# Kernel tuning notes

Hardware: AMD Instinct MI355X
Metric: run time of the kernel (lower is better)

Reference implementation:

```python
import jax, jax.numpy as jnp
import numpy as np

K = 3        # patch size (size=(3,3))
DIL = 1      # dilation
EPS = 1e-8


def _unfold(x, k=K, d=DIL):
    """im2col identical to torch.nn.Unfold(kernel_size=k, dilation=d).
    x: [N, C, H, W] -> [N, C*k*k, L], channel-major then (kh, kw) ordering."""
    N, C, H, W = x.shape
    Ho = H - d * (k - 1)
    Wo = W - d * (k - 1)
    rows = []
    for i in range(k):
        cols = [x[:, :, i * d:i * d + Ho, j * d:j * d + Wo] for j in range(k)]
        rows.append(jnp.stack(cols, axis=2))  # [N, C, k, Ho, Wo]
    patches = jnp.stack(rows, axis=2)         # [N, C, k, k, Ho, Wo]
    return patches.reshape(N, C * k * k, Ho * Wo)


def setup_inputs() -> dict:
    key = jax.random.key(0)
    k1, k2 = jax.random.split(key)
    x = jax.random.normal(k1, (1, 256, 96, 96), dtype=jnp.float32)
    style = jax.random.normal(k2, (1, 256, 96, 96), dtype=jnp.float32)
    return {"x": x, "style": style}


def reference(x, style):
    # Patches of input and style feature maps: [B, D, L] with D = C*3*3.
    ip = _unfold(x)       # [B, D, Li]
    sp = _unfold(style)   # [B, D, Ls]  (precomputed in __init__ in the torch module)

    # Normalized cross-correlation between every input patch and every style patch.
    ipn = ip / (jnp.linalg.norm(ip, axis=1, keepdims=True) + EPS)
    spn = sp / (jnp.linalg.norm(sp, axis=1, keepdims=True) + EPS)
    sim = jnp.einsum('bdi,bdj->bij', ipn, spn)  # [B, Li, Ls]

    # Nearest style patch for each input patch (Champandard patch matching).
    idx = jnp.argmax(sim, axis=2)                                  # [B, Li]
    matched = jnp.take_along_axis(sp, idx[:, None, :], axis=2)     # [B, D, Li]

    # MSE between input patches and their best-matching style patches.
    return jnp.mean((ip - matched) ** 2)
```

## Files before the change

### kernel.cpp

```cpp
#include <hip/hip_runtime.h>

#define CCH   256
#define HH    96
#define WW    96
#define HO    94
#define LL    8836
#define DD    2304
#define LPAD  8960

#define BM2   256
#define NT2   35
#define NPH   36
#define ASLB  16384
#define BBASEB 65536

typedef unsigned char u8;
typedef unsigned long long u64;

using i32x4 = __attribute__((ext_vector_type(4))) int;

#define OFF_BQ    20643840ull
#define OFF_RNB   41287680ull
#define OFF_N2B   41323520ull
#define OFF_W2X   41359360ull
#define OFF_QSA   41395200ull
#define OFF_QSB   41431040ull
#define OFF_COLS  41466880ull
#define OFF_SAF   41502720ull
#define OFF_P2    41538560ull
#define OFF_PM    41612288ull
#define OFF_BEST  41686016ull

__device__ __forceinline__ void gload16(const void* g, void* l) {
    __builtin_amdgcn_global_load_lds(
        (const __attribute__((address_space(1))) unsigned int*)g,
        (__attribute__((address_space(3))) unsigned int*)l,
        16, 0, 0);
}

__global__ __launch_bounds__(256) void k_chan_stats(const float* __restrict__ st,
                                                    const float* __restrict__ x,
                                                    float* __restrict__ P2,
                                                    float* __restrict__ PM) {
    int p = blockIdx.x * 256 + threadIdx.x;
    if (p >= 2 * HH * WW) return;
    const float* img = (p < HH * WW) ? st : x;
    int pp = (p < HH * WW) ? p : p - HH * WW;
    float s = 0.f, m = 0.f;
#pragma unroll 4
    for (int c = 0; c < CCH; ++c) {
        float v = img[c * (HH * WW) + pp];
        s += v * v;
        m = fmaxf(m, fabsf(v));
    }
    P2[p] = s;
    PM[p] = m;
}

__global__ __launch_bounds__(256) void k_win(const float* __restrict__ P2,
                                             const float* __restrict__ PM,
                                             float* __restrict__ rnB,
                                             float* __restrict__ n2B,
                                             float* __restrict__ win2x,
                                             float* __restrict__ qsA,
                                             float* __restrict__ qsB,
                                             float* __restrict__ colS,
                                             float* __restrict__ sAf) {
    int i = blockIdx.x * 256 + threadIdx.x;
    if (i >= LL) return;
    int y = i / HO, xc = i % HO;
    float ss = 0.f, sx = 0.f, ms = 0.f, mx = 0.f;
#pragma unroll
    for (int kh = 0; kh < 3; ++kh)
#pragma unroll
        for (int kw = 0; kw < 3; ++kw) {
            int off = (y + kh) * WW + xc + kw;
            ss += P2[off];
            sx += P2[HH * WW + off];
            ms = fmaxf(ms, PM[off]);
            mx = fmaxf(mx, PM[HH * WW + off]);
        }
    float rn = 1.f / (sqrtf(ss) + 1e-8f);
    float msc = fmaxf(ms, 1e-30f), mxc = fmaxf(mx, 1e-30f);
    rnB[i] = rn;
    n2B[i] = ss;
    win2x[i] = sx;
    qsA[i] = 127.f / mxc;
    qsB[i] = 127.f / msc;
    colS[i] = rn * msc * (1.f / 127.f);
    sAf[i] = mxc * (1.f / 127.f);
}

__global__ __launch_bounds__(512) void k_pack(const float* __restrict__ x,
                                              const float* __restrict__ st,
                                              const float* __restrict__ qsA,
                                              const float* __restrict__ qsB,
                                              u8* __restrict__ Aq,
                                              u8* __restrict__ Bq) {
    extern __shared__ u8 plds[];

    const int b = blockIdx.x;
    const int side = b & 1;
    const int half = (b >> 1) & 1;
    const int y = b >> 2;
    const int xc0 = half * 47;

    const float* src = side ? st : x;
    const float* qs  = side ? qsB : qsA;
    u8* dst = (side ? Bq : Aq) + (size_t)(y * HO + xc0) * DD;

    const int t = threadIdx.x;
    if (t < 47 * 9) {
        const int il = t / 9, k = t - il * 9;
        const int kh = k / 3, kw = k - kh * 3;
        const int i = y * HO + xc0 + il;
        const float scale = qs[i];
        const float* sp = src + (y + kh) * WW + (xc0 + il + kw);
        u8* lp = plds + il * DD + k;
#pragma unroll 8
        for (int c = 0; c < CCH; ++c) {
            int qv = (int)rintf(sp[c * (HH * WW)] * scale);
            lp[c * 9] = (u8)qv;
        }
    }
    __syncthreads();
    for (int idx = t; idx < 6768; idx += 512) {
        *(i32x4*)(dst + idx * 16) = *(const i32x4*)(plds + idx * 16);
    }
}

__global__ __launch_bounds__(512, 2) void k_gemm2(const u8* __restrict__ A,
                                                  const u8* __restrict__ Bm,
                                                  const float* __restrict__ colS,
                                                  u64* __restrict__ best) {
    extern __shared__ __align__(16) u8 lds[];

    const int t = threadIdx.x;
    const int wid = t >> 6, lane = t & 63;
    const int wr = wid >> 2, wc = wid & 3;
    const int l15 = lane & 15, l4 = lane >> 4;

    const int nwg = NT2 * NT2;
    const int q = nwg >> 3, r = nwg & 7;
    const int bid = blockIdx.x;
    const int xcd = bid & 7, loc = bid >> 3;
    const int swz = ((xcd < r) ? xcd * (q + 1) : r * (q + 1) + (xcd - r) * q) + loc;
    const int it = swz / NT2, jt = swz % NT2;

    const int gsrc = (t & 3) ^ ((t >> 3) & 3);
    const u8* pA0 = A  + (size_t)(it * BM2 + (t >> 2)) * DD + gsrc * 16;
    const u8* pB0 = Bm + (size_t)(jt * BM2 + (t >> 2)) * DD + gsrc * 16;

    const int sp16 = (l4 ^ ((l15 >> 1) & 3)) * 16;
    int aoff[8], boff[4];
#pragma unroll
    for (int mi = 0; mi < 8; ++mi)
        aoff[mi] = (wr * 128 + mi * 16 + l15) * 64 + sp16;
#pragma unroll
    for (int ni = 0; ni < 4; ++ni)
        boff[ni] = BBASEB + (wc * 64 + ni * 16 + l15) * 64 + sp16;

    i32x4 acc[8][4];
#pragma unroll
    for (int mi = 0; mi < 8; ++mi)
#pragma unroll
        for (int ni = 0; ni < 4; ++ni)
            acc[mi][ni] = (i32x4){0, 0, 0, 0};

#define PSTAGE(S)                                                            \
    do {                                                                     \
        const u8* sa = pA0 + (size_t)(S) * 64;                               \
        const u8* sb = pB0 + (size_t)(S) * 64;                               \
        gload16(sa,          lds + (S) * ASLB + t * 16);                     \
        gload16(sa + 294912, lds + (S) * ASLB + 8192 + t * 16);              \
        gload16(sb,          lds + BBASEB + (S) * ASLB + t * 16);            \
        gload16(sb + 294912, lds + BBASEB + (S) * ASLB + 8192 + t * 16);     \
    } while (0)
    PSTAGE(0); PSTAGE(1); PSTAGE(2);
#undef PSTAGE
    asm volatile("s_waitcnt vmcnt(8)" ::: "memory");
    __builtin_amdgcn_sched_barrier(0);
    __builtin_amdgcn_s_barrier();

    i32x4 af03[4], af47[4], bfr[4];

#define SUBA(U)                                                              \
    {                                                                        \
        _Pragma("unroll")                                                    \
        for (int ni = 0; ni < 4; ++ni)                                       \
            bfr[ni] = *(const i32x4*)(lds + (U) * ASLB + boff[ni]);          \
        _Pragma("unroll")                                                    \
        for (int mi = 0; mi < 4; ++mi)                                       \
            af03[mi] = *(const i32x4*)(lds + (U) * ASLB + aoff[mi]);         \
        {                                                                    \
            const int ss = (kb + (U) + 3 > NPH - 1) ? (NPH - 1) : (kb + (U) + 3); \
            const u8* sa = pA0 + (size_t)ss * 64;                            \
            u8* da = lds + (((U) + 3) & 3) * ASLB + t * 16;                  \
            gload16(sa,          da);                                        \
            gload16(sa + 294912, da + 8192);                                 \
        }                                                                    \
        __builtin_amdgcn_s_barrier();                                        \
        asm volatile("s_waitcnt lgkmcnt(0)" ::: "memory");                   \
        __builtin_amdgcn_sched_barrier(0);                                   \
        __builtin_amdgcn_s_setprio(1);                                       \
        _Pragma("unroll")                                                    \
        for (int mi = 0; mi < 4; ++mi)                                       \
            _Pragma("unroll")                                                \
            for (int ni = 0; ni < 4; ++ni)                                   \
                acc[mi][ni] = __builtin_amdgcn_mfma_i32_16x16x64_i8(         \
                    af03[mi], bfr[ni], acc[mi][ni], 0, 0, 0);                \
        __builtin_amdgcn_s_setprio(0);                                       \
        __builtin_amdgcn_s_barrier();                                        \
    }

#define SUBB(U)                                                              \
    {                                                                        \
        _Pragma("unroll")                                                    \
        for (int mi = 0; mi < 4; ++mi)                                       \
            af47[mi] = *(const i32x4*)(lds + (U) * ASLB + aoff[4 + mi]);     \
        {                                                                    \
            const int ss = (kb + (U) + 3 > NPH - 1) ? (NPH - 1) : (kb + (U) + 3); \
            const u8* sb = pB0 + (size_t)ss * 64;                            \
            u8* db = lds + BBASEB + (((U) + 3) & 3) * ASLB + t * 16;         \
            gload16(sb,          db);                                       \
            gload16(sb + 294912, db + 8192);                                 \
        }                                                                    \
        asm volatile("s_waitcnt vmcnt(8)" ::: "memory");                     \
        __builtin_amdgcn_sched_barrier(0);                                   \
        __builtin_amdgcn_s_barrier();                                        \
        asm volatile("s_waitcnt lgkmcnt(0)" ::: "memory");                   \
        __builtin_amdgcn_sched_barrier(0);                                   \
        __builtin_amdgcn_s_setprio(1);                                       \
        _Pragma("unroll")                                                    \
        for (int mi = 0; mi < 4; ++mi)                                       \
            _Pragma("unroll")                                                \
            for (int ni = 0; ni < 4; ++ni)                                   \
                acc[4 + mi][ni] = __builtin_amdgcn_mfma_i32_16x16x64_i8(     \
                    af47[mi], bfr[ni], acc[4 + mi][ni], 0, 0, 0);            \
        __builtin_amdgcn_s_setprio(0);                                       \
        __builtin_amdgcn_s_barrier();                                        \
    }

    for (int kt = 0; kt < NPH / 4; ++kt) {
        const int kb = kt * 4;
        SUBA(0) SUBB(0)
        SUBA(1) SUBB(1)
        SUBA(2) SUBB(2)
        SUBA(3) SUBB(3)
    }
#undef SUBA
#undef SUBB

    const int jbase = jt * BM2 + wc * 64 + l15;
    float cs[4];
#pragma unroll
    for (int ni = 0; ni < 4; ++ni) {
        int j = jbase + ni * 16;
        cs[ni] = colS[j < LL ? j : 0];
    }
#pragma unroll
    for (int mi = 0; mi < 8; ++mi) {
#pragma unroll
        for (int rr = 0; rr < 4; ++rr) {
            float bv = -3.4e38f;
            int bj = 0x7FFFFFFF;
#pragma unroll
            for (int ni = 0; ni < 4; ++ni) {
                int j = jbase + ni * 16;
                float v = (float)acc[mi][ni][rr] * cs[ni];
                if (j < LL && (v > bv || (v == bv && j < bj))) { bv = v; bj = j; }
            }
#pragma unroll
            for (int m = 1; m < 16; m <<= 1) {
                float ov = __shfl_xor(bv, m, 64);
                int oj = __shfl_xor(bj, m, 64);
                if (ov > bv || (ov == bv && oj < bj)) { bv = ov; bj = oj; }
            }
            if (l15 == 0) {
                int i = it * BM2 + wr * 128 + mi * 16 + l4 * 4 + rr;
                if (i < LL) {
                    unsigned u = __float_as_uint(bv);
                    unsigned s = (bv < 0.f) ? ~u : (u | 0x80000000u);
                    u64 packed = ((u64)s << 32) | (unsigned)(~(unsigned)bj);
                    atomicMax(&best[i], packed);
                }
            }
        }
    }
}

__global__ __launch_bounds__(256) void k_final(const u64* __restrict__ best,
                                               const float* __restrict__ rnB,
                                               const float* __restrict__ n2B,
                                               const float* __restrict__ win2x,
                                               const float* __restrict__ sAf,
                                               float* __restrict__ out) {
    int i = blockIdx.x * 256 + threadIdx.x;
    float contrib = 0.f;
    if (i < LL) {
        u64 p = best[i];
        unsigned s = (unsigned)(p >> 32);
        unsigned ub = (s & 0x80000000u) ? (s & 0x7FFFFFFFu) : ~s;
        float bv = __uint_as_float(ub);
        int j = (int)(~(unsigned)(p & 0xFFFFFFFFull));
        float dot = (bv * sAf[i]) / rnB[j];
        contrib = win2x[i] + n2B[j] - 2.f * dot;
    }
    float sred = contrib;
#pragma unroll
    for (int o = 32; o > 0; o >>= 1) sred += __shfl_down(sred, o, 64);
    __shared__ float red[4];
    if ((threadIdx.x & 63) == 0) red[threadIdx.x >> 6] = sred;
    __syncthreads();
    if (threadIdx.x == 0) {
        float tot = red[0] + red[1] + red[2] + red[3];
        atomicAdd(out, tot * (1.0f / ((float)DD * (float)LL)));
    }
}

extern "C" void kernel_launch(void* const* d_in, const int* in_sizes, int n_in,
                              void* d_out, int out_size, void* d_ws, size_t ws_size,
                              hipStream_t stream) {
    const float* x  = (const float*)d_in[0];
    const float* st = (const float*)d_in[1];
    char* ws = (char*)d_ws;

    u8* Aq       = (u8*)ws;
    u8* Bq       = (u8*)(ws + OFF_BQ);
    float* rnB   = (float*)(ws + OFF_RNB);
    float* n2B   = (float*)(ws + OFF_N2B);
    float* win2x = (float*)(ws + OFF_W2X);
    float* qsA   = (float*)(ws + OFF_QSA);
    float* qsB   = (float*)(ws + OFF_QSB);
    float* colS  = (float*)(ws + OFF_COLS);
    float* sAf   = (float*)(ws + OFF_SAF);
    float* P2    = (float*)(ws + OFF_P2);
    float* PM    = (float*)(ws + OFF_PM);
    u64* best    = (u64*)(ws + OFF_BEST);
    float* out   = (float*)d_out;

    hipFuncSetAttribute((const void*)k_gemm2,
                        hipFuncAttributeMaxDynamicSharedMemorySize, 131072);
    hipFuncSetAttribute((const void*)k_pack,
                        hipFuncAttributeMaxDynamicSharedMemorySize, 110592);

    hipMemsetAsync(best, 0, (size_t)LL * 8, stream);
    hipMemsetAsync(out, 0, sizeof(float), stream);
    hipMemsetAsync(Aq + (size_t)LL * DD, 0, (size_t)(LPAD - LL) * DD, stream);
    hipMemsetAsync(Bq + (size_t)LL * DD, 0, (size_t)(LPAD - LL) * DD, stream);

    k_chan_stats<<<dim3(72), dim3(256), 0, stream>>>(st, x, P2, PM);
    k_win<<<dim3(35), dim3(256), 0, stream>>>(P2, PM, rnB, n2B, win2x, qsA, qsB, colS, sAf);
    k_pack<<<dim3(HO * 4), dim3(512), 108288, stream>>>(x, st, qsA, qsB, Aq, Bq);
    k_gemm2<<<dim3(NT2 * NT2), dim3(512), 131072, stream>>>(Aq, Bq, colS, best);
    k_final<<<dim3(35), dim3(256), 0, stream>>>(best, rnB, n2B, win2x, sAf, out);
}
```

Baseline: 400.0 us.

## Halve GEMM M-tile, use 3-stage LDS pipeline, fold memsets into k_win

The int8 MFMA similarity GEMM moves from 256x256 tiles with a 4-stage split A/B prefetch to 128x256 tiles with a simpler 3-stage ring buffer. This cuts LDS to 72KB and accumulators to 16 per lane, so more blocks can be resident and latency is hidden better. The cost is less data reuse per tile and more global traffic for B. The best-index and output memsets are now done inside k_win, and the zeroing of the padded rows is dropped, which saves several async launches. Padded rows are safe only because their results are masked by the i<LL and j<LL checks.

```diff
diff --git a/kernel.cpp b/kernel.cpp
--- a/kernel.cpp
+++ b/kernel.cpp
@@ -8,11 +8,10 @@
 #define DD    2304
 #define LPAD  8960
 
-#define BM2   256
-#define NT2   35
+#define NTI   70
+#define NTJ   35
 #define NPH   36
-#define ASLB  16384
-#define BBASEB 65536
+#define SLTB  24576
 
 typedef unsigned char u8;
 typedef unsigned long long u64;
@@ -65,9 +64,13 @@
                                              float* __restrict__ qsA,
                                              float* __restrict__ qsB,
                                              float* __restrict__ colS,
-                                             float* __restrict__ sAf) {
+                                             float* __restrict__ sAf,
+                                             u64* __restrict__ best,
+                                             float* __restrict__ out) {
     int i = blockIdx.x * 256 + threadIdx.x;
     if (i >= LL) return;
+    if (i == 0) *out = 0.f;
+    best[i] = 0;
     int y = i / HO, xc = i % HO;
     float ss = 0.f, sx = 0.f, ms = 0.f, mx = 0.f;
 #pragma unroll
@@ -129,7 +132,7 @@
     }
 }
 
-__global__ __launch_bounds__(512, 2) void k_gemm2(const u8* __restrict__ A,
+__global__ __launch_bounds__(512, 4) void k_gemm2(const u8* __restrict__ A,
                                                   const u8* __restrict__ Bm,
                                                   const float* __restrict__ colS,
                                                   u64* __restrict__ best) {
@@ -140,65 +143,63 @@
     const int wr = wid >> 2, wc = wid & 3;
     const int l15 = lane & 15, l4 = lane >> 4;
 
-    const int nwg = NT2 * NT2;
+    const int nwg = NTI * NTJ;
     const int q = nwg >> 3, r = nwg & 7;
     const int bid = blockIdx.x;
     const int xcd = bid & 7, loc = bid >> 3;
     const int swz = ((xcd < r) ? xcd * (q + 1) : r * (q + 1) + (xcd - r) * q) + loc;
-    const int it = swz / NT2, jt = swz % NT2;
+    const int it = swz / NTJ, jt = swz % NTJ;
 
     const int gsrc = (t & 3) ^ ((t >> 3) & 3);
-    const u8* pA0 = A  + (size_t)(it * BM2 + (t >> 2)) * DD + gsrc * 16;
-    const u8* pB0 = Bm + (size_t)(jt * BM2 + (t >> 2)) * DD + gsrc * 16;
+    const u8* srcA = A  + (size_t)(it * 128 + (t >> 2)) * DD + gsrc * 16;
+    const u8* srcB = Bm + (size_t)(jt * 256 + (t >> 2)) * DD + gsrc * 16;
 
     const int sp16 = (l4 ^ ((l15 >> 1) & 3)) * 16;
-    int aoff[8], boff[4];
-#pragma unroll
-    for (int mi = 0; mi < 8; ++mi)
-        aoff[mi] = (wr * 128 + mi * 16 + l15) * 64 + sp16;
+    int aoff[4], boff[4];
+#pragma unroll
+    for (int mi = 0; mi < 4; ++mi)
+        aoff[mi] = (wr * 64 + mi * 16 + l15) * 64 + sp16;
 #pragma unroll
     for (int ni = 0; ni < 4; ++ni)
-        boff[ni] = BBASEB + (wc * 64 + ni * 16 + l15) * 64 + sp16;
-
-    i32x4 acc[8][4];
-#pragma unroll
-    for (int mi = 0; mi < 8; ++mi)
+        boff[ni] = 8192 + (wc * 64 + ni * 16 + l15) * 64 + sp16;
+
+    i32x4 acc[4][4];
+#pragma unroll
+    for (int mi = 0; mi < 4; ++mi)
 #pragma unroll
         for (int ni = 0; ni < 4; ++ni)
             acc[mi][ni] = (i32x4){0, 0, 0, 0};
 
-#define PSTAGE(S)                                                            \
+    i32x4 af[4], bf[4];
+
+#define STAGE(SS, SP)                                                        \
     do {                                                                     \
-        const u8* sa = pA0 + (size_t)(S) * 64;                               \
-        const u8* sb = pB0 + (size_t)(S) * 64;                               \
-        gload16(sa,          lds + (S) * ASLB + t * 16);                     \
-        gload16(sa + 294912, lds + (S) * ASLB + 8192 + t * 16);              \
-        gload16(sb,          lds + BBASEB + (S) * ASLB + t * 16);            \
-        gload16(sb + 294912, lds + BBASEB + (S) * ASLB + 8192 + t * 16);     \
+        const int sc_ = ((SS) > NPH - 1) ? (NPH - 1) : (SS);                 \
+        const u8* sa = srcA + (size_t)sc_ * 64;                              \
+        const u8* sb = srcB + (size_t)sc_ * 64;                              \
+        u8* d = lds + (SP) * SLTB + t * 16;                                  \
+        gload16(sa, d);                                                      \
+        gload16(sb, d + 8192);                                               \
+        gload16(sb + 128 * DD, d + 16384);                                   \
     } while (0)
-    PSTAGE(0); PSTAGE(1); PSTAGE(2);
-#undef PSTAGE
-    asm volatile("s_waitcnt vmcnt(8)" ::: "memory");
+
+    STAGE(0, 0);
+    STAGE(1, 1);
+    asm volatile("s_waitcnt vmcnt(3)" ::: "memory");
     __builtin_amdgcn_sched_barrier(0);
     __builtin_amdgcn_s_barrier();
 
-    i32x4 af03[4], af47[4], bfr[4];
-
-#define SUBA(U)                                                              \
+#define BODY(S, SC, SP)                                                      \
     {                                                                        \
         _Pragma("unroll")                                                    \
         for (int ni = 0; ni < 4; ++ni)                                       \
-            bfr[ni] = *(const i32x4*)(lds + (U) * ASLB + boff[ni]);          \
+            bf[ni] = *(const i32x4*)(lds + (SC) * SLTB + boff[ni]);          \
         _Pragma("unroll")                                                    \
         for (int mi = 0; mi < 4; ++mi)                                       \
-            af03[mi] = *(const i32x4*)(lds + (U) * ASLB + aoff[mi]);         \
-        {                                                                    \
-            const int ss = (kb + (U) + 3 > NPH - 1) ? (NPH - 1) : (kb + (U) + 3); \
-            const u8* sa = pA0 + (size_t)ss * 64;                            \
-            u8* da = lds + (((U) + 3) & 3) * ASLB + t * 16;                  \
-            gload16(sa,          da);                                        \
-            gload16(sa + 294912, da + 8192);                                 \
-        }                                                                    \
+            af[mi] = *(const i32x4*)(lds + (SC) * SLTB + aoff[mi]);          \
+        STAGE((S) + 2, SP);                                                  \
+        asm volatile("s_waitcnt vmcnt(3)" ::: "memory");                     \
+        __builtin_amdgcn_sched_barrier(0);                                   \
         __builtin_amdgcn_s_barrier();                                        \
         asm volatile("s_waitcnt lgkmcnt(0)" ::: "memory");                   \
         __builtin_amdgcn_sched_barrier(0);                                   \
@@ -208,50 +209,20 @@
             _Pragma("unroll")                                                \
             for (int ni = 0; ni < 4; ++ni)                                   \
                 acc[mi][ni] = __builtin_amdgcn_mfma_i32_16x16x64_i8(         \
-                    af03[mi], bfr[ni], acc[mi][ni], 0, 0, 0);                \
+                    af[mi], bf[ni], acc[mi][ni], 0, 0, 0);                   \
         __builtin_amdgcn_s_setprio(0);                                       \
         __builtin_amdgcn_s_barrier();                                        \
     }
 
-#define SUBB(U)                                                              \
-    {                                                                        \
-        _Pragma("unroll")                                                    \
-        for (int mi = 0; mi < 4; ++mi)                                       \
-            af47[mi] = *(const i32x4*)(lds + (U) * ASLB + aoff[4 + mi]);     \
-        {                                                                    \
-            const int ss = (kb + (U) + 3 > NPH - 1) ? (NPH - 1) : (kb + (U) + 3); \
-            const u8* sb = pB0 + (size_t)ss * 64;                            \
-            u8* db = lds + BBASEB + (((U) + 3) & 3) * ASLB + t * 16;         \
-            gload16(sb,          db);                                       \
-            gload16(sb + 294912, db + 8192);                                 \
-        }                                                                    \
-        asm volatile("s_waitcnt vmcnt(8)" ::: "memory");                     \
-        __builtin_amdgcn_sched_barrier(0);                                   \
-        __builtin_amdgcn_s_barrier();                                        \
-        asm volatile("s_waitcnt lgkmcnt(0)" ::: "memory");                   \
-        __builtin_amdgcn_sched_barrier(0);                                   \
-        __builtin_amdgcn_s_setprio(1);                                       \
-        _Pragma("unroll")                                                    \
-        for (int mi = 0; mi < 4; ++mi)                                       \
-            _Pragma("unroll")                                                \
-            for (int ni = 0; ni < 4; ++ni)                                   \
-                acc[4 + mi][ni] = __builtin_amdgcn_mfma_i32_16x16x64_i8(     \
-                    af47[mi], bfr[ni], acc[4 + mi][ni], 0, 0, 0);            \
-        __builtin_amdgcn_s_setprio(0);                                       \
-        __builtin_amdgcn_s_barrier();                                        \
-    }
-
-    for (int kt = 0; kt < NPH / 4; ++kt) {
-        const int kb = kt * 4;
-        SUBA(0) SUBB(0)
-        SUBA(1) SUBB(1)
-        SUBA(2) SUBB(2)
-        SUBA(3) SUBB(3)
-    }
-#undef SUBA
-#undef SUBB
-
-    const int jbase = jt * BM2 + wc * 64 + l15;
+    for (int s3 = 0; s3 < NPH; s3 += 3) {
+        BODY(s3,     0, 2)
+        BODY(s3 + 1, 1, 0)
+        BODY(s3 + 2, 2, 1)
+    }
+#undef BODY
+#undef STAGE
+
+    const int jbase = jt * 256 + wc * 64 + l15;
     float cs[4];
 #pragma unroll
     for (int ni = 0; ni < 4; ++ni) {
@@ -259,7 +230,7 @@
         cs[ni] = colS[j < LL ? j : 0];
     }
 #pragma unroll
-    for (int mi = 0; mi < 8; ++mi) {
+    for (int mi = 0; mi < 4; ++mi) {
 #pragma unroll
         for (int rr = 0; rr < 4; ++rr) {
             float bv = -3.4e38f;
@@ -277,7 +248,7 @@
                 if (ov > bv || (ov == bv && oj < bj)) { bv = ov; bj = oj; }
             }
             if (l15 == 0) {
-                int i = it * BM2 + wr * 128 + mi * 16 + l4 * 4 + rr;
+                int i = it * 128 + wr * 64 + mi * 16 + l4 * 4 + rr;
                 if (i < LL) {
                     unsigned u = __float_as_uint(bv);
                     unsigned s = (bv < 0.f) ? ~u : (u | 0x80000000u);
@@ -340,18 +311,14 @@
     float* out   = (float*)d_out;
 
     hipFuncSetAttribute((const void*)k_gemm2,
-                        hipFuncAttributeMaxDynamicSharedMemorySize, 131072);
+                        hipFuncAttributeMaxDynamicSharedMemorySize, 73728);
     hipFuncSetAttribute((const void*)k_pack,
                         hipFuncAttributeMaxDynamicSharedMemorySize, 110592);
 
-    hipMemsetAsync(best, 0, (size_t)LL * 8, stream);
-    hipMemsetAsync(out, 0, sizeof(float), stream);
-    hipMemsetAsync(Aq + (size_t)LL * DD, 0, (size_t)(LPAD - LL) * DD, stream);
-    hipMemsetAsync(Bq + (size_t)LL * DD, 0, (size_t)(LPAD - LL) * DD, stream);
-
     k_chan_stats<<<dim3(72), dim3(256), 0, stream>>>(st, x, P2, PM);
-    k_win<<<dim3(35), dim3(256), 0, stream>>>(P2, PM, rnB, n2B, win2x, qsA, qsB, colS, sAf);
+    k_win<<<dim3(35), dim3(256), 0, stream>>>(P2, PM, rnB, n2B, win2x,
+                                              qsA, qsB, colS, sAf, best, out);
     k_pack<<<dim3(HO * 4), dim3(512), 108288, stream>>>(x, st, qsA, qsB, Aq, Bq);
-    k_gemm2<<<dim3(NT2 * NT2), dim3(512), 131072, stream>>>(Aq, Bq, colS, best);
+    k_gemm2<<<dim3(NTI * NTJ), dim3(512), 73728, stream>>>(Aq, Bq, colS, best);
     k_final<<<dim3(35), dim3(256), 0, stream>>>(best, rnB, n2B, win2x, sAf, out);
 }
```

Measured after the change: 351.0 us. -12.2%, faster.
